# Optimization experiments

Hardware: AMD Instinct MI355X
Metric: run time of the kernel (lower is better)

The kernel has to match this reference:

```python
import jax, jax.numpy as jnp
import numpy as np

N, E, B = 20000, 320000, 16
DIN, HID, HEADS, ZDIM = 128, 128, 4, 128
NEG_SLOPE = 0.2


def _glorot(key, shape):
    fan = sum(shape[-2:]) if len(shape) >= 2 else shape[-1] * 2
    return jax.random.normal(key, shape, jnp.float32) * jnp.sqrt(2.0 / fan)


def setup_inputs() -> dict:
    key = jax.random.key(0)
    ks = jax.random.split(key, 20)
    inp = {
        "x": jax.random.normal(ks[0], (N, DIN), jnp.float32),
        "edge_index": jax.random.randint(ks[1], (2, E), 0, N),
        "batch_id": jnp.sort(jax.random.randint(ks[2], (N,), 0, B)),
        "node_mask": jax.random.bernoulli(ks[3], 0.1, (N,)),
        "edge_mask": jax.random.bernoulli(ks[4], 0.5, (E,)),
    }
    # layer dims: e_Fs=[128,128,128,128]; heads=4 on layers 0,1; heads=1 last
    dims = [(DIN, HID, HEADS), (HID * HEADS, HID, HEADS), (HID * HEADS, ZDIM, 1)]
    for li, (fin, fout, h) in enumerate(dims, start=1):
        inp[f"W{li}"] = _glorot(ks[4 + 3 * li], (fin, h * fout))
        inp[f"att_src{li}"] = _glorot(ks[5 + 3 * li], (h, fout))
        inp[f"att_dst{li}"] = _glorot(ks[6 + 3 * li], (h, fout))
        inp[f"bias{li}"] = jnp.zeros((h * fout,), jnp.float32)
    return inp


def _gat_layer(x, W, a_src, a_dst, bias, src, dst, heads, fout):
    n = x.shape[0]
    h = (x @ W).reshape(n, heads, fout)            # [N,H,F]
    alpha_s = (h * a_src).sum(-1)                  # [N,H]
    alpha_d = (h * a_dst).sum(-1)                  # [N,H]
    e = jax.nn.leaky_relu(alpha_s[src] + alpha_d[dst], NEG_SLOPE)  # [E,H]
    m = jax.ops.segment_max(e, dst, num_segments=n)
    ex = jnp.exp(e - m[dst])
    denom = jax.ops.segment_sum(ex, dst, num_segments=n)
    w = ex / denom[dst]                            # segment softmax over incoming edges
    out = jax.ops.segment_sum(h[src] * w[:, :, None], dst, num_segments=n)  # [N,H,F]
    return out.reshape(n, heads * fout) + bias


def reference(x, edge_index, batch_id, node_mask, edge_mask,
              W1, att_src1, att_dst1, bias1,
              W2, att_src2, att_dst2, bias2,
              W3, att_src3, att_dst3, bias3):
    n = x.shape[0]
    loop = jnp.arange(n)
    src = jnp.concatenate([edge_index[0], loop])   # add_self_loops=True
    dst = jnp.concatenate([edge_index[1], loop])
    # edge_mask is passed as edge_attr but GATConv has edge_dim=None -> ignored
    h = _gat_layer(x, W1, att_src1, att_dst1, bias1, src, dst, HEADS, HID)
    h = jax.nn.relu(h)
    h = _gat_layer(h, W2, att_src2, att_dst2, bias2, src, dst, HEADS, HID)
    h = jax.nn.relu(h)
    h = _gat_layer(h, W3, att_src3, att_dst3, bias3, src, dst, 1, ZDIM)
    # masked global max pool: if mask.sum()>0 pool over ~mask else all nodes
    has_masked = jnp.any(node_mask)
    valid = jnp.logical_or(~node_mask, ~has_masked)
    neg = jnp.asarray(-1e30, h.dtype)
    vals = jnp.where(valid[:, None], h, neg)
    return jax.ops.segment_max(vals, batch_id, num_segments=B)
```

## Files before the change

### kernel.cpp

```cpp
#include <hip/hip_runtime.h>
#include <stdint.h>


#define NN 20000
#define MPAD 20480
#define NE 320000
#define NBATCH 16
#define NEG 0.2f
#define WSCALE 64.0f
#define WINV 0.015625f

using f16x8 = __attribute__((ext_vector_type(8))) _Float16;
using f32x4 = __attribute__((ext_vector_type(4))) float;
using h2 = __attribute__((ext_vector_type(2))) _Float16;

#define GLL16(gp, lp)                                                        \
  __builtin_amdgcn_global_load_lds(                                          \
      (const __attribute__((address_space(1))) void*)(gp),                   \
      (__attribute__((address_space(3))) void*)(lp), 16, 0, 0)

static __device__ __forceinline__ unsigned short h2u(_Float16 h) {
  union { _Float16 f; unsigned short u; } c;
  c.f = h;
  return c.u;
}
static __device__ __forceinline__ h2 bits2h2(unsigned v) {
  union { unsigned u; h2 h; } c;
  c.u = v;
  return c.h;
}
static __device__ __forceinline__ unsigned h22bits(h2 h) {
  union { h2 h; unsigned u; } c;
  c.h = h;
  return c.u;
}
static __device__ __forceinline__ unsigned encf(float f) {
  unsigned u = __float_as_uint(f);
  return (u & 0x80000000u) ? ~u : (u | 0x80000000u);
}
static __device__ __forceinline__ float decf(unsigned u) {
  return __uint_as_float((u & 0x80000000u) ? (u ^ 0x80000000u) : ~u);
}

#define R1 (512 * 128)
#define R2 (512 * 512)
#define R3 (128 * 512)
#define PREPTOT (R1 + R2 + R3 + NN * 128)
__global__ void k_init_prep(const float* __restrict__ W1, const float* __restrict__ W2,
                            const float* __restrict__ W3, const float* __restrict__ x,
                            unsigned short* __restrict__ wt1,
                            unsigned short* __restrict__ wt2,
                            unsigned short* __restrict__ wt3,
                            unsigned short* __restrict__ xp, int* deg,
                            unsigned* enc, int* flag, float* alz, int alcount) {
  int idx = blockIdx.x * blockDim.x + threadIdx.x;
  if (idx < R1) {
    int n = idx & 511, k = idx >> 9;
    wt1[(size_t)n * 128 + k] = h2u((_Float16)(W1[(size_t)k * 512 + n] * WSCALE));
  } else if (idx < R1 + R2) {
    int j = idx - R1;
    int n = j & 511, k = j >> 9;
    wt2[(size_t)n * 512 + k] = h2u((_Float16)(W2[(size_t)k * 512 + n] * WSCALE));
  } else if (idx < R1 + R2 + R3) {
    int j = idx - (R1 + R2);
    int n = j & 127, k = j >> 7;
    wt3[(size_t)n * 512 + k] = h2u((_Float16)(W3[(size_t)k * 128 + n] * WSCALE));
  } else if (idx < PREPTOT) {
    int j = idx - (R1 + R2 + R3);
    xp[j] = h2u((_Float16)x[j]);
  }
  if (idx < NN) deg[idx] = 1;
  if (idx < NBATCH * 128) enc[idx] = ~__float_as_uint(-1e30f);
  if (idx == 0) *flag = 0;
  if (idx < alcount) alz[idx] = 0.f;
}

__global__ void k_count(const int* __restrict__ ei, int* __restrict__ deg) {
  int e = blockIdx.x * blockDim.x + threadIdx.x;
  if (e < NE) atomicAdd(&deg[ei[NE + e]], 1);
}

__global__ void k_scan(const int* __restrict__ deg, int* __restrict__ row_ptr,
                       int* __restrict__ cursor) {
  __shared__ int wsum[16];
  int t = threadIdx.x;
  int lane = t & 63, wid = t >> 6;
  const int CH = 20;
  int beg = t * CH;
  int s = 0;
  for (int i = 0; i < CH; i++) {
    int idx = beg + i;
    if (idx < NN) s += deg[idx];
  }
  int incl = s;
  for (int off = 1; off < 64; off <<= 1) {
    int v = __shfl_up(incl, off, 64);
    if (lane >= off) incl += v;
  }
  if (lane == 63) wsum[wid] = incl;
  __syncthreads();
  if (t < 16) {
    int v = wsum[t];
    int in2 = v;
    for (int off = 1; off < 16; off <<= 1) {
      int u = __shfl_up(in2, off, 16);
      if (t >= off) in2 += u;
    }
    wsum[t] = in2 - v;
  }
  __syncthreads();
  int run = wsum[wid] + incl - s;
  for (int i = 0; i < CH; i++) {
    int idx = beg + i;
    if (idx < NN) {
      row_ptr[idx] = run;
      cursor[idx] = run;
      run += deg[idx];
    }
  }
  if (t == 1023) row_ptr[NN] = run;
}

__global__ void k_fill(const int* __restrict__ ei, int* __restrict__ cursor,
                       int* __restrict__ col, const int* __restrict__ nmask,
                       int* __restrict__ flag) {
  int i = blockIdx.x * blockDim.x + threadIdx.x;
  if (i >= NE + NN) return;
  int src, dst;
  if (i < NE) {
    src = ei[i];
    dst = ei[NE + i];
  } else {
    src = dst = i - NE;
    if (nmask[src] != 0) *flag = 1;
  }
  int pos = atomicAdd(&cursor[dst], 1);
  col[pos] = src;
}

#define BN 128
#define BK 32

template <int BMT, int NT, bool SWIZ>
__global__ __launch_bounds__(NT, 4) void k_gemm(
    const unsigned short* __restrict__ Ap, const unsigned short* __restrict__ Wt,
    unsigned short* __restrict__ C, const float* __restrict__ attS,
    const float* __restrict__ attD, float* __restrict__ alS,
    float* __restrict__ alD, int K, int Nc, int H) {
  __shared__ __align__(16) unsigned short As[BMT][BK];
  __shared__ __align__(16) unsigned short Bs[BN][BK];
  int tid = threadIdx.x;
  int bm, bn;
  if constexpr (SWIZ) {
    int id = blockIdx.x;
    int r = id & 7, t = id >> 3;
    bn = (t & 3) * BN;
    bm = (((t >> 2) << 3) + r) * BMT;
  } else {
    bm = blockIdx.y * BMT;
    bn = blockIdx.x * BN;
  }
  int wid = tid >> 6, lane = tid & 63;
  int wm = (BMT == 128) ? (wid >> 1) * 64 : 0;
  int wn = (BMT == 128) ? (wid & 1) * 64 : wid * 64;
  int lrow = lane & 15, lquad = lane >> 4;

  f32x4 acc[4][4] = {};

  for (int k0 = 0; k0 < K; k0 += BK) {
    __syncthreads();
#pragma unroll
    for (int i = 0; i < (BMT * 4) / NT; i++) {
      int slot = tid + NT * i;
      int row = slot >> 2;
      int ks = (slot & 3) * 8;
      GLL16(Ap + (size_t)(bm + row) * K + k0 + ks, &As[0][0] + (size_t)slot * 8);
    }
#pragma unroll
    for (int i = 0; i < 512 / NT; i++) {
      int slot = tid + NT * i;
      int row = slot >> 2;
      int ks = (slot & 3) * 8;
      GLL16(Wt + (size_t)(bn + row) * K + k0 + ks, &Bs[0][0] + (size_t)slot * 8);
    }
    __syncthreads();

    f16x8 af[4];
#pragma unroll
    for (int mf = 0; mf < 4; mf++)
      af[mf] = *(const f16x8*)&As[wm + mf * 16 + lrow][lquad * 8];
#pragma unroll
    for (int nf = 0; nf < 4; nf++) {
      f16x8 bf = *(const f16x8*)&Bs[wn + nf * 16 + lrow][lquad * 8];
#pragma unroll
      for (int mf = 0; mf < 4; mf++)
        acc[mf][nf] =
            __builtin_amdgcn_mfma_f32_16x16x32_f16(bf, af[mf], acc[mf][nf], 0, 0, 0);
    }
  }
#pragma unroll
  for (int mf = 0; mf < 4; mf++)
#pragma unroll
    for (int nf = 0; nf < 4; nf++)
#pragma unroll
      for (int r = 0; r < 4; r++) acc[mf][nf][r] *= WINV;

  float4 aS[4], aD[4];
#pragma unroll
  for (int nf = 0; nf < 4; nf++) {
    int n0 = bn + wn + nf * 16 + lquad * 4;
    aS[nf] = *(const float4*)(attS + n0);
    aD[nf] = *(const float4*)(attD + n0);
  }
  int head = bn >> 7;
#pragma unroll
  for (int mf = 0; mf < 4; mf++) {
    float ps = 0.f, pd = 0.f;
#pragma unroll
    for (int nf = 0; nf < 4; nf++) {
      ps += acc[mf][nf][0] * aS[nf].x + acc[mf][nf][1] * aS[nf].y +
            acc[mf][nf][2] * aS[nf].z + acc[mf][nf][3] * aS[nf].w;
      pd += acc[mf][nf][0] * aD[nf].x + acc[mf][nf][1] * aD[nf].y +
            acc[mf][nf][2] * aD[nf].z + acc[mf][nf][3] * aD[nf].w;
    }
    ps += __shfl_xor(ps, 16, 64);
    ps += __shfl_xor(ps, 32, 64);
    pd += __shfl_xor(pd, 16, 64);
    pd += __shfl_xor(pd, 32, 64);
    int row = bm + wm + mf * 16 + lrow;
    if (lquad == 0) {
      atomicAdd(&alS[(size_t)row * H + head], ps);
      atomicAdd(&alD[(size_t)row * H + head], pd);
    }
  }
#pragma unroll
  for (int mf = 0; mf < 4; mf++) {
    int m = bm + wm + mf * 16 + lrow;
#pragma unroll
    for (int nf = 0; nf < 4; nf++) {
      int n0 = bn + wn + nf * 16 + lquad * 4;
      ushort4 o;
      o.x = h2u((_Float16)acc[mf][nf][0]);
      o.y = h2u((_Float16)acc[mf][nf][1]);
      o.z = h2u((_Float16)acc[mf][nf][2]);
      o.w = h2u((_Float16)acc[mf][nf][3]);
      *(ushort4*)(C + (size_t)m * Nc + n0) = o;
    }
  }
}

template <int H, bool RELU, bool FP16OUT, bool PIN>
__global__ __launch_bounds__(256) void k_agg(
    const unsigned short* __restrict__ h, const float* __restrict__ as_,
    const float* __restrict__ ad_, const int* __restrict__ row_ptr,
    const int* __restrict__ col, const float* __restrict__ bias,
    float* __restrict__ out, unsigned short* __restrict__ outp) {
  constexpr int HF = H * 128;
  __shared__ unsigned long long cw[4][64];
  int tid = threadIdx.x, bwid = tid >> 6, lane = tid & 63;
  int node, sub;
  if constexpr (PIN) {
    sub = blockIdx.x & 3;
    node = (blockIdx.x >> 2) * 4 + bwid;
  } else {
    node = blockIdx.x * 4 + bwid;
    sub = 0;
    if (node >= NN) return;
  }
  int beg = row_ptr[node], end = row_ptr[node + 1];
  int deg = end - beg;
  float adv = ad_[(size_t)node * H + sub];
  float shift = (adv > 0.f) ? adv : NEG * adv;
  float fscale = 1.f;
  bool fast = (deg <= 64);

  if (__builtin_expect(fast, 1)) {
    unsigned sidx = 0;
    float t = 0.f;
    if (lane < deg) {
      sidx = (unsigned)col[beg + lane];
      float e = as_[(size_t)sidx * H + sub] + adv;
      e = (e > 0.f) ? e : NEG * e;
      t = fminf(__expf(e - shift), 60000.f);
    }
    _Float16 ht = (_Float16)t;
    h2 hv;
    hv[0] = ht;
    hv[1] = ht;
    cw[bwid][lane] = ((unsigned long long)h22bits(hv) << 32) | sidx;
    float S = t;
#pragma unroll
    for (int off = 32; off; off >>= 1) S += __shfl_xor(S, off, 64);
    fscale = 1.f / S;
  }
  float Mr = 0.f, Sinv = 0.f;
  if (!fast) {
    float m = -1e30f, s = 0.f;
    for (int j = beg + lane; j < end; j += 64) {
      int sidx = col[j];
      float e = as_[(size_t)sidx * H + sub] + adv;
      e = (e > 0.f) ? e : NEG * e;
      float nm = fmaxf(m, e);
      s = s * __expf(m - nm) + __expf(e - nm);
      m = nm;
    }
    float mm = m;
#pragma unroll
    for (int off = 32; off; off >>= 1) mm = fmaxf(mm, __shfl_xor(mm, off, 64));
    float t = s * __expf(m - mm);
#pragma unroll
    for (int off = 32; off; off >>= 1) t += __shfl_xor(t, off, 64);
    Mr = mm;
    Sinv = 1.f / t;
  }

  const int half = lane >> 5, hl = lane & 31;
  const int fbase = sub * 128 + hl * 4;
  const int base = half * 8;
  float acc0 = 0.f, acc1 = 0.f, acc2 = 0.f, acc3 = 0.f;
  for (int c0 = beg; c0 < end; c0 += 64) {
    int cnt = min(64, end - c0);
    if (!fast) {
      unsigned sidx = 0;
      float w = 0.f;
      if (lane < cnt) {
        sidx = (unsigned)col[c0 + lane];
        float e = as_[(size_t)sidx * H + sub] + adv;
        e = (e > 0.f) ? e : NEG * e;
        w = __expf(e - Mr) * Sinv;
      }
      _Float16 hw = (_Float16)w;
      h2 hv;
      hv[0] = hw;
      hv[1] = hw;
      cw[bwid][lane] = ((unsigned long long)h22bits(hv) << 32) | sidx;
    }
    h2 hacc0 = {(_Float16)0.f, (_Float16)0.f};
    h2 hacc1 = {(_Float16)0.f, (_Float16)0.f};
    for (int je = 0; je < cnt; je += 16) {
      unsigned long long q[8];
#pragma unroll
      for (int r = 0; r < 8; r++) q[r] = cw[bwid][je + base + r];
      uint2 v[8];
#pragma unroll
      for (int r = 0; r < 8; r++)
        v[r] = *(const uint2*)(h + (size_t)(unsigned)q[r] * HF + fbase);
#pragma unroll
      for (int r = 0; r < 8; r++) {
        h2 hw = bits2h2((unsigned)(q[r] >> 32));
        hacc0 += hw * bits2h2(v[r].x);
        hacc1 += hw * bits2h2(v[r].y);
      }
    }
    acc0 += (float)hacc0[0];
    acc1 += (float)hacc0[1];
    acc2 += (float)hacc1[0];
    acc3 += (float)hacc1[1];
  }
  acc0 += __shfl_xor(acc0, 32, 64);
  acc1 += __shfl_xor(acc1, 32, 64);
  acc2 += __shfl_xor(acc2, 32, 64);
  acc3 += __shfl_xor(acc3, 32, 64);
  if (half == 0) {
    float4 b = *(const float4*)(bias + fbase);
    float v0 = acc0 * fscale + b.x, v1 = acc1 * fscale + b.y;
    float v2 = acc2 * fscale + b.z, v3 = acc3 * fscale + b.w;
    if (RELU) {
      v0 = fmaxf(v0, 0.f);
      v1 = fmaxf(v1, 0.f);
      v2 = fmaxf(v2, 0.f);
      v3 = fmaxf(v3, 0.f);
    }
    if constexpr (FP16OUT) {
      ushort4 o;
      o.x = h2u((_Float16)v0);
      o.y = h2u((_Float16)v1);
      o.z = h2u((_Float16)v2);
      o.w = h2u((_Float16)v3);
      *(ushort4*)(outp + (size_t)node * HF + fbase) = o;
    } else {
      float4 o = make_float4(v0, v1, v2, v3);
      *(float4*)(out + (size_t)node * HF + fbase) = o;
    }
  }
}

__global__ void k_pool(const float* __restrict__ h, const int* __restrict__ batch,
                       const int* __restrict__ mask, const int* __restrict__ flag,
                       unsigned* __restrict__ enc) {
  int f = threadIdx.x;
  int n0 = blockIdx.x * 32;
  if (n0 >= NN) return;
  int n1 = min(NN, n0 + 32);
  int any = *flag;
  float local = -1e30f;
  int curb = batch[n0];
  for (int n = n0; n < n1; ++n) {
    int b = batch[n];
    if (b != curb) {
      if (local > -1e30f) atomicMax(&enc[curb * 128 + f], encf(local));
      local = -1e30f;
      curb = b;
    }
    bool valid = (mask[n] == 0) || (!any);
    if (valid) local = fmaxf(local, h[(size_t)n * 128 + f]);
  }
  if (local > -1e30f) atomicMax(&enc[curb * 128 + f], encf(local));
}

__global__ void k_out(const unsigned* __restrict__ enc, float* __restrict__ out) {
  int i = blockIdx.x * blockDim.x + threadIdx.x;
  if (i < NBATCH * 128) out[i] = decf(enc[i]);
}

extern "C" void kernel_launch(void* const* d_in, const int* in_sizes, int n_in,
                              void* d_out, int out_size, void* d_ws, size_t ws_size,
                              hipStream_t stream) {
  const float* x = (const float*)d_in[0];
  const int* ei = (const int*)d_in[1];
  const int* batch = (const int*)d_in[2];
  const int* nmask = (const int*)d_in[3];
  const float* W1 = (const float*)d_in[5];
  const float* as1 = (const float*)d_in[6];
  const float* ad1 = (const float*)d_in[7];
  const float* b1 = (const float*)d_in[8];
  const float* W2 = (const float*)d_in[9];
  const float* as2 = (const float*)d_in[10];
  const float* ad2 = (const float*)d_in[11];
  const float* b2 = (const float*)d_in[12];
  const float* W3 = (const float*)d_in[13];
  const float* as3 = (const float*)d_in[14];
  const float* ad3 = (const float*)d_in[15];
  const float* b3 = (const float*)d_in[16];

  char* ws = (char*)d_ws;
  size_t off = 0;
  auto alloc = [&](size_t bytes) -> char* {
    char* p = ws + off;
    off = (off + bytes + 255) & ~(size_t)255;
    return p;
  };
  unsigned short* hA = (unsigned short*)alloc((size_t)MPAD * 512 * 2);
  unsigned short* hG = (unsigned short*)alloc((size_t)MPAD * 512 * 2);
  float* out3 = (float*)alloc((size_t)MPAD * 128 * 4);
  unsigned short* xP = (unsigned short*)out3;
  unsigned short* wt1 = (unsigned short*)alloc((size_t)512 * 128 * 2);
  unsigned short* wt2 = (unsigned short*)alloc((size_t)512 * 512 * 2);
  unsigned short* wt3 = (unsigned short*)alloc((size_t)128 * 512 * 2);
  char* alStart = ws + off;
  float* alS1 = (float*)alloc((size_t)MPAD * 4 * 4);
  float* alD1 = (float*)alloc((size_t)MPAD * 4 * 4);
  float* alS2 = (float*)alloc((size_t)MPAD * 4 * 4);
  float* alD2 = (float*)alloc((size_t)MPAD * 4 * 4);
  float* alS3 = (float*)alloc((size_t)MPAD * 4);
  float* alD3 = (float*)alloc((size_t)MPAD * 4);
  int alcount = (int)(((ws + off) - alStart) / 4);
  int* deg = (int*)alloc((size_t)NN * 4);
  int* cursor = (int*)alloc((size_t)NN * 4);
  int* rowp = (int*)alloc((size_t)(NN + 1) * 4);
  int* colx = (int*)alloc((size_t)(NE + NN) * 4);
  unsigned* enc = (unsigned*)alloc((size_t)NBATCH * 128 * 4);
  int* flag = (int*)alloc(4);
  (void)ws_size; (void)n_in; (void)in_sizes; (void)out_size;

  k_init_prep<<<(PREPTOT + 255) / 256, 256, 0, stream>>>(
      W1, W2, W3, x, wt1, wt2, wt3, xP, deg, enc, flag, (float*)alStart, alcount);
  k_count<<<(NE + 255) / 256, 256, 0, stream>>>(ei, deg);
  k_scan<<<1, 1024, 0, stream>>>(deg, rowp, cursor);
  k_fill<<<(NE + NN + 255) / 256, 256, 0, stream>>>(ei, cursor, colx, nmask, flag);

  const int gemmBlocks = 4 * (MPAD / 128);
  dim3 gg3(1, MPAD / 64);

  k_gemm<128, 256, true><<<gemmBlocks, 256, 0, stream>>>(
      xP, wt1, hA, as1, ad1, alS1, alD1, 128, 512, 4);
  k_agg<4, true, true, true><<<NN, 256, 0, stream>>>(hA, alS1, alD1, rowp, colx,
                                                     b1, nullptr, hG);
  k_gemm<128, 256, true><<<gemmBlocks, 256, 0, stream>>>(
      hG, wt2, hA, as2, ad2, alS2, alD2, 512, 512, 4);
  k_agg<4, true, true, true><<<NN, 256, 0, stream>>>(hA, alS2, alD2, rowp, colx,
                                                     b2, nullptr, hG);
  k_gemm<64, 128, false><<<gg3, 128, 0, stream>>>(hG, wt3, hA, as3, ad3, alS3,
                                                  alD3, 512, 128, 1);
  k_agg<1, false, false, false><<<(NN + 3) / 4, 256, 0, stream>>>(
      hA, alS3, alD3, rowp, colx, b3, out3, nullptr);

  k_pool<<<(NN + 31) / 32, 128, 0, stream>>>(out3, batch, nmask, flag, enc);
  k_out<<<(NBATCH * 128 + 255) / 256, 256, 0, stream>>>(enc, (float*)d_out);
}
```

Before: 346.2 us.

## Widen aggregation gathers to 16-byte loads and store last-layer output in fp16

The aggregation kernel now has each lane gather 8 fp16 features (a uint4) per neighbor, with four edge groups per wavefront instead of two halves, and reduces the partial sums across lanes with two shuffles. The intent is fewer, wider memory transactions on the neighbor feature gather, which dominates the kernel. The last layer now writes fp16 output, and the pooling kernel reads it as fp16, which halves that traffic. This lowers the precision of the final pooled values.

```diff
diff --git a/kernel.cpp b/kernel.cpp
--- a/kernel.cpp
+++ b/kernel.cpp
@@ -23,6 +23,11 @@
   union { _Float16 f; unsigned short u; } c;
   c.f = h;
   return c.u;
+}
+static __device__ __forceinline__ float u2f(unsigned short u) {
+  union { unsigned short u; _Float16 f; } c;
+  c.u = u;
+  return (float)c.f;
 }
 static __device__ __forceinline__ h2 bits2h2(unsigned v) {
   union { unsigned u; h2 h; } c;
@@ -314,10 +319,10 @@
     Sinv = 1.f / t;
   }
 
-  const int half = lane >> 5, hl = lane & 31;
-  const int fbase = sub * 128 + hl * 4;
-  const int base = half * 8;
-  float acc0 = 0.f, acc1 = 0.f, acc2 = 0.f, acc3 = 0.f;
+  const int se = lane >> 4;
+  const int fb = sub * 128 + (lane & 15) * 8;
+  const unsigned short* __restrict__ hb = h + fb;
+  float facc[8] = {0.f, 0.f, 0.f, 0.f, 0.f, 0.f, 0.f, 0.f};
   for (int c0 = beg; c0 < end; c0 += 64) {
     int cnt = min(64, end - c0);
     if (!fast) {
@@ -335,57 +340,85 @@
       hv[1] = hw;
       cw[bwid][lane] = ((unsigned long long)h22bits(hv) << 32) | sidx;
     }
-    h2 hacc0 = {(_Float16)0.f, (_Float16)0.f};
-    h2 hacc1 = {(_Float16)0.f, (_Float16)0.f};
-    for (int je = 0; je < cnt; je += 16) {
+    h2 ha0 = {(_Float16)0.f, (_Float16)0.f};
+    h2 ha1 = ha0, ha2 = ha0, ha3 = ha0;
+    for (int je = 0; je < cnt; je += 32) {
+      int ng = (cnt - je + 3) >> 2;
+      if (ng > 8) ng = 8;
       unsigned long long q[8];
-#pragma unroll
-      for (int r = 0; r < 8; r++) q[r] = cw[bwid][je + base + r];
-      uint2 v[8];
+      uint4 v[8];
 #pragma unroll
       for (int r = 0; r < 8; r++)
-        v[r] = *(const uint2*)(h + (size_t)(unsigned)q[r] * HF + fbase);
-#pragma unroll
-      for (int r = 0; r < 8; r++) {
-        h2 hw = bits2h2((unsigned)(q[r] >> 32));
-        hacc0 += hw * bits2h2(v[r].x);
-        hacc1 += hw * bits2h2(v[r].y);
-      }
-    }
-    acc0 += (float)hacc0[0];
-    acc1 += (float)hacc0[1];
-    acc2 += (float)hacc1[0];
-    acc3 += (float)hacc1[1];
-  }
-  acc0 += __shfl_xor(acc0, 32, 64);
-  acc1 += __shfl_xor(acc1, 32, 64);
-  acc2 += __shfl_xor(acc2, 32, 64);
-  acc3 += __shfl_xor(acc3, 32, 64);
-  if (half == 0) {
-    float4 b = *(const float4*)(bias + fbase);
-    float v0 = acc0 * fscale + b.x, v1 = acc1 * fscale + b.y;
-    float v2 = acc2 * fscale + b.z, v3 = acc3 * fscale + b.w;
+        if (r < ng) {
+          q[r] = cw[bwid][je + se + 4 * r];
+          v[r] = *(const uint4*)(hb + (size_t)(unsigned)q[r] * HF);
+        }
+#pragma unroll
+      for (int r = 0; r < 8; r++)
+        if (r < ng) {
+          h2 hw = bits2h2((unsigned)(q[r] >> 32));
+          ha0 += hw * bits2h2(v[r].x);
+          ha1 += hw * bits2h2(v[r].y);
+          ha2 += hw * bits2h2(v[r].z);
+          ha3 += hw * bits2h2(v[r].w);
+        }
+    }
+    facc[0] += (float)ha0[0];
+    facc[1] += (float)ha0[1];
+    facc[2] += (float)ha1[0];
+    facc[3] += (float)ha1[1];
+    facc[4] += (float)ha2[0];
+    facc[5] += (float)ha2[1];
+    facc[6] += (float)ha3[0];
+    facc[7] += (float)ha3[1];
+  }
+#pragma unroll
+  for (int k = 0; k < 8; k++) {
+    facc[k] += __shfl_xor(facc[k], 16, 64);
+    facc[k] += __shfl_xor(facc[k], 32, 64);
+  }
+  if (lane < 16) {
+    float4 b0 = *(const float4*)(bias + fb);
+    float4 b1 = *(const float4*)(bias + fb + 4);
+    float v0 = facc[0] * fscale + b0.x, v1 = facc[1] * fscale + b0.y;
+    float v2 = facc[2] * fscale + b0.z, v3 = facc[3] * fscale + b0.w;
+    float v4 = facc[4] * fscale + b1.x, v5 = facc[5] * fscale + b1.y;
+    float v6 = facc[6] * fscale + b1.z, v7 = facc[7] * fscale + b1.w;
     if (RELU) {
       v0 = fmaxf(v0, 0.f);
       v1 = fmaxf(v1, 0.f);
       v2 = fmaxf(v2, 0.f);
       v3 = fmaxf(v3, 0.f);
+      v4 = fmaxf(v4, 0.f);
+      v5 = fmaxf(v5, 0.f);
+      v6 = fmaxf(v6, 0.f);
+      v7 = fmaxf(v7, 0.f);
     }
     if constexpr (FP16OUT) {
-      ushort4 o;
-      o.x = h2u((_Float16)v0);
-      o.y = h2u((_Float16)v1);
-      o.z = h2u((_Float16)v2);
-      o.w = h2u((_Float16)v3);
-      *(ushort4*)(outp + (size_t)node * HF + fbase) = o;
+      h2 p0, p1, p2, p3;
+      p0[0] = (_Float16)v0;
+      p0[1] = (_Float16)v1;
+      p1[0] = (_Float16)v2;
+      p1[1] = (_Float16)v3;
+      p2[0] = (_Float16)v4;
+      p2[1] = (_Float16)v5;
+      p3[0] = (_Float16)v6;
+      p3[1] = (_Float16)v7;
+      uint4 o;
+      o.x = h22bits(p0);
+      o.y = h22bits(p1);
+      o.z = h22bits(p2);
+      o.w = h22bits(p3);
+      *(uint4*)(outp + (size_t)node * HF + fb) = o;
     } else {
-      float4 o = make_float4(v0, v1, v2, v3);
-      *(float4*)(out + (size_t)node * HF + fbase) = o;
-    }
-  }
-}
-
-__global__ void k_pool(const float* __restrict__ h, const int* __restrict__ batch,
+      *(float4*)(out + (size_t)node * HF + fb) = make_float4(v0, v1, v2, v3);
+      *(float4*)(out + (size_t)node * HF + fb + 4) = make_float4(v4, v5, v6, v7);
+    }
+  }
+}
+
+__global__ void k_pool(const unsigned short* __restrict__ h,
+                       const int* __restrict__ batch,
                        const int* __restrict__ mask, const int* __restrict__ flag,
                        unsigned* __restrict__ enc) {
   int f = threadIdx.x;
@@ -403,7 +436,7 @@
       curb = b;
     }
     bool valid = (mask[n] == 0) || (!any);
-    if (valid) local = fmaxf(local, h[(size_t)n * 128 + f]);
+    if (valid) local = fmaxf(local, u2f(h[(size_t)n * 128 + f]));
   }
   if (local > -1e30f) atomicMax(&enc[curb * 128 + f], encf(local));
 }
@@ -444,6 +477,7 @@
   unsigned short* hG = (unsigned short*)alloc((size_t)MPAD * 512 * 2);
   float* out3 = (float*)alloc((size_t)MPAD * 128 * 4);
   unsigned short* xP = (unsigned short*)out3;
+  unsigned short* out3h = (unsigned short*)out3;
   unsigned short* wt1 = (unsigned short*)alloc((size_t)512 * 128 * 2);
   unsigned short* wt2 = (unsigned short*)alloc((size_t)512 * 512 * 2);
   unsigned short* wt3 = (unsigned short*)alloc((size_t)128 * 512 * 2);
@@ -482,9 +516,9 @@
                                                      b2, nullptr, hG);
   k_gemm<64, 128, false><<<gg3, 128, 0, stream>>>(hG, wt3, hA, as3, ad3, alS3,
                                                   alD3, 512, 128, 1);
-  k_agg<1, false, false, false><<<(NN + 3) / 4, 256, 0, stream>>>(
-      hA, alS3, alD3, rowp, colx, b3, out3, nullptr);
-
-  k_pool<<<(NN + 31) / 32, 128, 0, stream>>>(out3, batch, nmask, flag, enc);
+  k_agg<1, false, true, false><<<(NN + 3) / 4, 256, 0, stream>>>(
+      hA, alS3, alD3, rowp, colx, b3, nullptr, out3h);
+
+  k_pool<<<(NN + 31) / 32, 128, 0, stream>>>(out3h, batch, nmask, flag, enc);
   k_out<<<(NBATCH * 128 + 255) / 256, 256, 0, stream>>>(enc, (float*)d_out);
 }
```

New measurement: 389.0 us. +12.4%, slower.
